# Kernel tuning notes

Hardware: AMD Instinct MI355X
Metric: run time of the kernel (lower is better)

Reference implementation:

```python
import jax, jax.numpy as jnp
import numpy as np

L_COORD = 5.0
L_NOOBJ = 0.5
S = 7  # YOLOv1 grid size


def _iou(b1, b2):
    # b1, b2: [..., 4] = (cx, cy, w, h), centers expressed in grid-cell units (divide by S)
    x1 = b1[..., 0] / S - b1[..., 2] / 2
    y1 = b1[..., 1] / S - b1[..., 3] / 2
    x2 = b1[..., 0] / S + b1[..., 2] / 2
    y2 = b1[..., 1] / S + b1[..., 3] / 2
    u1 = b2[..., 0] / S - b2[..., 2] / 2
    v1 = b2[..., 1] / S - b2[..., 3] / 2
    u2 = b2[..., 0] / S + b2[..., 2] / 2
    v2 = b2[..., 1] / S + b2[..., 3] / 2
    a1 = (x2 - x1) * (y2 - y1)
    a2 = (u2 - u1) * (v2 - v1)
    left = jnp.maximum(x1, u1)
    right = jnp.minimum(x2, u2)
    top = jnp.maximum(y1, v1)
    bottom = jnp.minimum(y2, v2)
    valid = (left < right) & (top < bottom)
    inter = jnp.where(valid, (right - left) * (bottom - top), 0.0)
    union = a1 + a2 - inter
    return jnp.where(valid, inter / union, 0.0)


def _yolo_loss(predict, label):
    # predict, label: [N, 7, 7, 26]; layout = [box1(5), box2(5), classes(16)]
    N = predict.shape[0]
    conf_lab = label[..., 4]
    coord_m = (conf_lab > 0).astype(predict.dtype)   # cells with an object
    noobj_m = (conf_lab == 0).astype(predict.dtype)  # empty cells

    # no-object cells: both predicted confidences pushed to 0
    noobj_c = jnp.sum(noobj_m * (predict[..., 4] ** 2 + predict[..., 9] ** 2))

    # class MSE on object cells
    class_loss = jnp.sum(coord_m * jnp.sum((predict[..., 10:] - label[..., 10:]) ** 2, axis=-1))

    b1 = predict[..., 0:4]
    c1 = predict[..., 4]
    b2 = predict[..., 5:9]
    c2 = predict[..., 9]
    lb = label[..., 0:4]

    iou1 = _iou(b1, lb)
    iou2 = _iou(b2, lb)
    pick1 = iou1 > iou2  # responsible box (strict >, matching torch)

    sel = jnp.where(pick1[..., None], b1, b2)  # select responsible box before sqrt
    coord_cell = (jnp.sum((sel[..., :2] - lb[..., :2]) ** 2, axis=-1)
                  + jnp.sum((jnp.sqrt(sel[..., 2:4]) - jnp.sqrt(lb[..., 2:4])) ** 2, axis=-1))
    obj_c_cell = jnp.where(pick1, (c1 - iou1) ** 2, (c2 - iou2) ** 2)
    noobj_extra = jnp.where(pick1, c2 ** 2, c1 ** 2)  # non-responsible box conf -> 0

    coord_loss = jnp.sum(coord_m * coord_cell)
    obj_c_loss = jnp.sum(coord_m * obj_c_cell)
    noobj_c = noobj_c + jnp.sum(coord_m * noobj_extra)

    return (L_COORD * coord_loss + obj_c_loss + L_NOOBJ * noobj_c + class_loss) / N


def setup_inputs() -> dict:
    key = jax.random.key(0)
    k1, k2, k3 = jax.random.split(key, 3)
    B = 8192
    # positive values so sqrt(w), sqrt(h) are well-defined (as the torch code assumes)
    predict = jax.random.uniform(k1, (B, 7, 7, 26), jnp.float32, 0.05, 1.0)
    label = jax.random.uniform(k2, (B, 7, 7, 26), jnp.float32, 0.05, 1.0)
    obj = (jax.random.uniform(k3, (B, 7, 7)) < 0.04).astype(jnp.float32)  # ~2 objects/image
    label = label.at[..., 4].set(obj)
    return {"predict": predict, "label": label}


def reference(predict, label):
    return _yolo_loss(predict, label)
```

## Files before the change

kernel.cpp:

```cpp
#include <hip/hip_runtime.h>

#define NCH 26
#define CPB 256
#define THREADS 256
#define TILE_FLOATS (CPB * NCH)
#define TILE_BYTES  (TILE_FLOATS * 4)

typedef __attribute__((address_space(3))) unsigned int  lds_u32_t;
typedef const __attribute__((address_space(1))) unsigned int glb_u32_t;

__device__ __forceinline__ float iou_pair_r(const float* b, const float* g) {
    const float inv_s = 1.0f / 7.0f;
    float x1 = b[0] * inv_s - b[2] * 0.5f;
    float y1 = b[1] * inv_s - b[3] * 0.5f;
    float x2 = b[0] * inv_s + b[2] * 0.5f;
    float y2 = b[1] * inv_s + b[3] * 0.5f;
    float u1 = g[0] * inv_s - g[2] * 0.5f;
    float v1 = g[1] * inv_s - g[3] * 0.5f;
    float u2 = g[0] * inv_s + g[2] * 0.5f;
    float v2 = g[1] * inv_s + g[3] * 0.5f;
    float a1 = (x2 - x1) * (y2 - y1);
    float a2 = (u2 - u1) * (v2 - v1);
    float left   = fmaxf(x1, u1);
    float right  = fminf(x2, u2);
    float top    = fmaxf(y1, v1);
    float bottom = fminf(y2, v2);
    bool valid = (left < right) && (top < bottom);
    float inter = valid ? (right - left) * (bottom - top) : 0.0f;
    float uni = a1 + a2 - inter;
    return valid ? inter / uni : 0.0f;
}

__global__ __launch_bounds__(THREADS) void yolo_loss_main(
        const float* __restrict__ predict,
        const float* __restrict__ label,
        float* __restrict__ partials,
        int n_cells) {
    __shared__ float sp[TILE_FLOATS];
    __shared__ float sl[TILE_FLOATS];

    const int tid = threadIdx.x;
    const int bid = blockIdx.x;
    const int wave = tid >> 6;
    const int lane = tid & 63;
    const long long base = (long long)bid * TILE_FLOATS;
    const long long total = (long long)n_cells * NCH;

    if (base + TILE_FLOATS <= total) {
        const char* gp = (const char*)(predict + base);
        const char* gl = (const char*)(label + base);
        #pragma unroll
        for (int c = 0; c < 7; ++c) {
            int chunk = wave + 4 * c;
            if (chunk < 26) {
                int off = chunk * 1024 + lane * 16;
                __builtin_amdgcn_global_load_lds(
                    (glb_u32_t*)(gp + off),
                    (lds_u32_t*)((char*)sp + off), 16, 0, 0);
                __builtin_amdgcn_global_load_lds(
                    (glb_u32_t*)(gl + off),
                    (lds_u32_t*)((char*)sl + off), 16, 0, 0);
            }
        }
    } else {
        for (int i = tid; i < TILE_FLOATS; i += THREADS) {
            long long g = base + i;
            sp[i] = (g < total) ? predict[g] : 0.0f;
            sl[i] = (g < total) ? label[g] : 0.0f;
        }
    }
    __syncthreads();

    float partial = 0.0f;
    long long cell = (long long)bid * CPB + tid;
    if (cell < n_cells) {
        float p[NCH], l[NCH];
        const float2* pv = (const float2*)&sp[tid * NCH];
        const float2* lv = (const float2*)&sl[tid * NCH];
        #pragma unroll
        for (int k = 0; k < 13; ++k) {
            float2 a = pv[k]; p[2 * k] = a.x; p[2 * k + 1] = a.y;
            float2 b = lv[k]; l[2 * k] = b.x; l[2 * k + 1] = b.y;
        }

        float conf_lab = l[4];
        float coord_m = (conf_lab > 0.0f) ? 1.0f : 0.0f;
        float noobj_m = (conf_lab == 0.0f) ? 1.0f : 0.0f;

        float acc_noobj = noobj_m * (p[4] * p[4] + p[9] * p[9]);

        float class_s = 0.0f;
        #pragma unroll
        for (int k = 10; k < 26; ++k) {
            float d = p[k] - l[k];
            class_s += d * d;
        }

        float iou1 = iou_pair_r(p + 0, l);
        float iou2 = iou_pair_r(p + 5, l);
        bool pick1 = iou1 > iou2;

        float s0 = pick1 ? p[0] : p[5];
        float s1 = pick1 ? p[1] : p[6];
        float s2 = pick1 ? p[2] : p[7];
        float s3 = pick1 ? p[3] : p[8];
        float dx = s0 - l[0];
        float dy = s1 - l[1];
        float dw = sqrtf(s2) - sqrtf(l[2]);
        float dh = sqrtf(s3) - sqrtf(l[3]);
        float coord_cell = dx * dx + dy * dy + dw * dw + dh * dh;

        float csel   = pick1 ? p[4] : p[9];
        float iousel = pick1 ? iou1 : iou2;
        float t = csel - iousel;
        float obj_c = t * t;

        float cother = pick1 ? p[9] : p[4];
        acc_noobj += coord_m * cother * cother;

        partial = 5.0f * coord_m * coord_cell
                + coord_m * obj_c
                + 0.5f * acc_noobj
                + coord_m * class_s;
    }

    #pragma unroll
    for (int off = 32; off > 0; off >>= 1)
        partial += __shfl_down(partial, off, 64);

    __shared__ float wsum[THREADS / 64];
    if ((tid & 63) == 0) wsum[tid >> 6] = partial;
    __syncthreads();
    if (tid == 0) {
        float s = 0.0f;
        #pragma unroll
        for (int w = 0; w < THREADS / 64; ++w) s += wsum[w];
        partials[bid] = s;
    }
}

__global__ __launch_bounds__(256) void yolo_loss_finalize(
        const float* __restrict__ partials, int n, float inv_n,
        float* __restrict__ out) {
    float s = 0.0f;
    for (int i = threadIdx.x; i < n; i += 256) s += partials[i];
    #pragma unroll
    for (int off = 32; off > 0; off >>= 1)
        s += __shfl_down(s, off, 64);
    __shared__ float wsum[4];
    if ((threadIdx.x & 63) == 0) wsum[threadIdx.x >> 6] = s;
    __syncthreads();
    if (threadIdx.x == 0)
        out[0] = (wsum[0] + wsum[1] + wsum[2] + wsum[3]) * inv_n;
}

extern "C" void kernel_launch(void* const* d_in, const int* in_sizes, int n_in,
                              void* d_out, int out_size, void* d_ws, size_t ws_size,
                              hipStream_t stream) {
    const float* predict = (const float*)d_in[0];
    const float* label   = (const float*)d_in[1];
    float* out = (float*)d_out;
    float* partials = (float*)d_ws;

    int total   = in_sizes[0];
    int n_cells = total / NCH;
    int N = n_cells / 49;
    int nblocks = (n_cells + CPB - 1) / CPB;

    yolo_loss_main<<<nblocks, THREADS, 0, stream>>>(predict, label, partials, n_cells);
    yolo_loss_finalize<<<1, 256, 0, stream>>>(partials, nblocks, 1.0f / (float)N, out);
}
```

Before: 101.5 us.

## Load labels directly to registers and fold finalize into atomic accumulation

Label data no longer goes through LDS. Each thread reads the label fields it needs straight from global memory into registers, skipping channels 5-9, which the loss never uses. This halves per-block LDS usage, which should let more blocks reside per CU and hide memory latency better. The separate finalize kernel is replaced by a memset plus per-block atomicAdd of the scaled partial, saving one launch but adding serialized atomics on a single address and a non-deterministic summation order.

Result: slower. 114.1 us (+12.4%).

```diff
diff --git a/kernel.cpp b/kernel.cpp
--- a/kernel.cpp
+++ b/kernel.cpp
@@ -4,7 +4,6 @@
 #define CPB 256
 #define THREADS 256
 #define TILE_FLOATS (CPB * NCH)
-#define TILE_BYTES  (TILE_FLOATS * 4)
 
 typedef __attribute__((address_space(3))) unsigned int  lds_u32_t;
 typedef const __attribute__((address_space(1))) unsigned int glb_u32_t;
@@ -34,10 +33,10 @@
 __global__ __launch_bounds__(THREADS) void yolo_loss_main(
         const float* __restrict__ predict,
         const float* __restrict__ label,
-        float* __restrict__ partials,
+        float* __restrict__ out,
+        float inv_n,
         int n_cells) {
     __shared__ float sp[TILE_FLOATS];
-    __shared__ float sl[TILE_FLOATS];
 
     const int tid = threadIdx.x;
     const int bid = blockIdx.x;
@@ -45,10 +44,10 @@
     const int lane = tid & 63;
     const long long base = (long long)bid * TILE_FLOATS;
     const long long total = (long long)n_cells * NCH;
+    const bool full_tile = (base + TILE_FLOATS <= total);
 
-    if (base + TILE_FLOATS <= total) {
+    if (full_tile) {
         const char* gp = (const char*)(predict + base);
-        const char* gl = (const char*)(label + base);
         #pragma unroll
         for (int c = 0; c < 7; ++c) {
             int chunk = wave + 4 * c;
@@ -57,30 +56,39 @@
                 __builtin_amdgcn_global_load_lds(
                     (glb_u32_t*)(gp + off),
                     (lds_u32_t*)((char*)sp + off), 16, 0, 0);
-                __builtin_amdgcn_global_load_lds(
-                    (glb_u32_t*)(gl + off),
-                    (lds_u32_t*)((char*)sl + off), 16, 0, 0);
             }
         }
     } else {
         for (int i = tid; i < TILE_FLOATS; i += THREADS) {
             long long g = base + i;
             sp[i] = (g < total) ? predict[g] : 0.0f;
-            sl[i] = (g < total) ? label[g] : 0.0f;
         }
     }
+
+    float l[NCH];
+    long long cell = (long long)bid * CPB + tid;
+    if (cell < n_cells) {
+        const float* lb = label + cell * NCH;
+        const float2* lv = (const float2*)lb;
+        float2 t0 = lv[0];  l[0] = t0.x; l[1] = t0.y;
+        float2 t1 = lv[1];  l[2] = t1.x; l[3] = t1.y;
+        l[4] = lb[4];
+        #pragma unroll
+        for (int k = 5; k < 13; ++k) {
+            float2 t = lv[k];
+            l[2 * k] = t.x; l[2 * k + 1] = t.y;
+        }
+    }
+
     __syncthreads();
 
     float partial = 0.0f;
-    long long cell = (long long)bid * CPB + tid;
     if (cell < n_cells) {
-        float p[NCH], l[NCH];
+        float p[NCH];
         const float2* pv = (const float2*)&sp[tid * NCH];
-        const float2* lv = (const float2*)&sl[tid * NCH];
         #pragma unroll
         for (int k = 0; k < 13; ++k) {
             float2 a = pv[k]; p[2 * k] = a.x; p[2 * k + 1] = a.y;
-            float2 b = lv[k]; l[2 * k] = b.x; l[2 * k + 1] = b.y;
         }
 
         float conf_lab = l[4];
@@ -135,23 +143,8 @@
         float s = 0.0f;
         #pragma unroll
         for (int w = 0; w < THREADS / 64; ++w) s += wsum[w];
-        partials[bid] = s;
+        atomicAdd(out, s * inv_n);
     }
-}
-
-__global__ __launch_bounds__(256) void yolo_loss_finalize(
-        const float* __restrict__ partials, int n, float inv_n,
-        float* __restrict__ out) {
-    float s = 0.0f;
-    for (int i = threadIdx.x; i < n; i += 256) s += partials[i];
-    #pragma unroll
-    for (int off = 32; off > 0; off >>= 1)
-        s += __shfl_down(s, off, 64);
-    __shared__ float wsum[4];
-    if ((threadIdx.x & 63) == 0) wsum[threadIdx.x >> 6] = s;
-    __syncthreads();
-    if (threadIdx.x == 0)
-        out[0] = (wsum[0] + wsum[1] + wsum[2] + wsum[3]) * inv_n;
 }
 
 extern "C" void kernel_launch(void* const* d_in, const int* in_sizes, int n_in,
@@ -160,13 +153,13 @@
     const float* predict = (const float*)d_in[0];
     const float* label   = (const float*)d_in[1];
     float* out = (float*)d_out;
-    float* partials = (float*)d_ws;
 
     int total   = in_sizes[0];
     int n_cells = total / NCH;
     int N = n_cells / 49;
     int nblocks = (n_cells + CPB - 1) / CPB;
 
-    yolo_loss_main<<<nblocks, THREADS, 0, stream>>>(predict, label, partials, n_cells);
-    yolo_loss_finalize<<<1, 256, 0, stream>>>(partials, nblocks, 1.0f / (float)N, out);
+    hipMemsetAsync(out, 0, sizeof(float) * out_size, stream);
+    yolo_loss_main<<<nblocks, THREADS, 0, stream>>>(
+        predict, label, out, 1.0f / (float)N, n_cells);
 }
```

## Use persistent single-wave blocks with double-buffered LDS prefetch of cell tiles

Applied to the files above, without the earlier changes.

Replaces the one-tile-per-block launch with a fixed grid of 768 single-wave blocks that loop over 128-cell tiles in grid-stride order. The next tile is prefetched into a second LDS buffer with direct global-to-LDS loads, waiting only for the current tile via vmcnt, so memory traffic overlaps with compute. Leftover cells are handled in the finalize kernel. It removes block-level syncthreads and per-block launch overhead, but each block has only one wave, so latency hiding depends on many resident blocks per CU and on the hand-written vmcnt count being correct.

New measurement: 105.9 us. 1.04x slower.

```diff
diff --git a/kernel.cpp b/kernel.cpp
--- a/kernel.cpp
+++ b/kernel.cpp
@@ -1,10 +1,9 @@
 #include <hip/hip_runtime.h>
 
 #define NCH 26
-#define CPB 256
-#define THREADS 256
-#define TILE_FLOATS (CPB * NCH)
-#define TILE_BYTES  (TILE_FLOATS * 4)
+#define TCELLS 128
+#define TILE_FLOATS (TCELLS * NCH)
+#define GRID_MAIN 768
 
 typedef __attribute__((address_space(3))) unsigned int  lds_u32_t;
 typedef const __attribute__((address_space(1))) unsigned int glb_u32_t;
@@ -31,119 +30,127 @@
     return valid ? inter / uni : 0.0f;
 }
 
-__global__ __launch_bounds__(THREADS) void yolo_loss_main(
+__device__ __forceinline__ float cell_loss(const float* p, const float* l) {
+    float conf_lab = l[4];
+    float coord_m = (conf_lab > 0.0f) ? 1.0f : 0.0f;
+    float noobj_m = (conf_lab == 0.0f) ? 1.0f : 0.0f;
+
+    float acc_noobj = noobj_m * (p[4] * p[4] + p[9] * p[9]);
+
+    float class_s = 0.0f;
+    #pragma unroll
+    for (int k = 10; k < 26; ++k) {
+        float d = p[k] - l[k];
+        class_s += d * d;
+    }
+
+    float iou1 = iou_pair_r(p + 0, l);
+    float iou2 = iou_pair_r(p + 5, l);
+    bool pick1 = iou1 > iou2;
+
+    float s0 = pick1 ? p[0] : p[5];
+    float s1 = pick1 ? p[1] : p[6];
+    float s2 = pick1 ? p[2] : p[7];
+    float s3 = pick1 ? p[3] : p[8];
+    float dx = s0 - l[0];
+    float dy = s1 - l[1];
+    float dw = sqrtf(s2) - sqrtf(l[2]);
+    float dh = sqrtf(s3) - sqrtf(l[3]);
+    float coord_cell = dx * dx + dy * dy + dw * dw + dh * dh;
+
+    float csel   = pick1 ? p[4] : p[9];
+    float iousel = pick1 ? iou1 : iou2;
+    float t = csel - iousel;
+    float obj_c = t * t;
+
+    float cother = pick1 ? p[9] : p[4];
+    acc_noobj += coord_m * cother * cother;
+
+    return 5.0f * coord_m * coord_cell
+         + coord_m * obj_c
+         + 0.5f * acc_noobj
+         + coord_m * class_s;
+}
+
+__global__ __launch_bounds__(64) void yolo_loss_main(
         const float* __restrict__ predict,
         const float* __restrict__ label,
         float* __restrict__ partials,
-        int n_cells) {
-    __shared__ float sp[TILE_FLOATS];
-    __shared__ float sl[TILE_FLOATS];
+        int n_tiles) {
+    __shared__ float lds[2][2][TILE_FLOATS];
+    const int lane = threadIdx.x;
+    const int bid  = blockIdx.x;
+    const int nb   = gridDim.x;
 
-    const int tid = threadIdx.x;
-    const int bid = blockIdx.x;
-    const int wave = tid >> 6;
-    const int lane = tid & 63;
-    const long long base = (long long)bid * TILE_FLOATS;
-    const long long total = (long long)n_cells * NCH;
-
-    if (base + TILE_FLOATS <= total) {
-        const char* gp = (const char*)(predict + base);
-        const char* gl = (const char*)(label + base);
+    auto stage = [&](int tile, int b) {
+        const char* gp = (const char*)(predict + (long long)tile * TILE_FLOATS);
+        const char* gl = (const char*)(label   + (long long)tile * TILE_FLOATS);
+        char* dp = (char*)&lds[b][0][0];
+        char* dl = (char*)&lds[b][1][0];
         #pragma unroll
-        for (int c = 0; c < 7; ++c) {
-            int chunk = wave + 4 * c;
-            if (chunk < 26) {
-                int off = chunk * 1024 + lane * 16;
-                __builtin_amdgcn_global_load_lds(
-                    (glb_u32_t*)(gp + off),
-                    (lds_u32_t*)((char*)sp + off), 16, 0, 0);
-                __builtin_amdgcn_global_load_lds(
-                    (glb_u32_t*)(gl + off),
-                    (lds_u32_t*)((char*)sl + off), 16, 0, 0);
-            }
+        for (int c = 0; c < 13; ++c) {
+            int off = c * 1024 + lane * 16;
+            __builtin_amdgcn_global_load_lds(
+                (glb_u32_t*)(gp + off), (lds_u32_t*)(dp + off), 16, 0, 0);
+            __builtin_amdgcn_global_load_lds(
+                (glb_u32_t*)(gl + off), (lds_u32_t*)(dl + off), 16, 0, 0);
         }
-    } else {
-        for (int i = tid; i < TILE_FLOATS; i += THREADS) {
-            long long g = base + i;
-            sp[i] = (g < total) ? predict[g] : 0.0f;
-            sl[i] = (g < total) ? label[g] : 0.0f;
-        }
-    }
-    __syncthreads();
+    };
 
     float partial = 0.0f;
-    long long cell = (long long)bid * CPB + tid;
-    if (cell < n_cells) {
-        float p[NCH], l[NCH];
-        const float2* pv = (const float2*)&sp[tid * NCH];
-        const float2* lv = (const float2*)&sl[tid * NCH];
+    int buf = 0;
+    if (bid < n_tiles) stage(bid, 0);
+
+    for (int t = bid; t < n_tiles; t += nb) {
+        int tn = t + nb;
+        if (tn < n_tiles) {
+            stage(tn, buf ^ 1);
+            asm volatile("s_waitcnt vmcnt(26)" ::: "memory");
+        } else {
+            asm volatile("s_waitcnt vmcnt(0)" ::: "memory");
+        }
+        __builtin_amdgcn_sched_barrier(0);
+
         #pragma unroll
-        for (int k = 0; k < 13; ++k) {
-            float2 a = pv[k]; p[2 * k] = a.x; p[2 * k + 1] = a.y;
-            float2 b = lv[k]; l[2 * k] = b.x; l[2 * k + 1] = b.y;
+        for (int h = 0; h < 2; ++h) {
+            int cell = lane + 64 * h;
+            float p[NCH], l[NCH];
+            const float2* pv = (const float2*)&lds[buf][0][cell * NCH];
+            const float2* lv = (const float2*)&lds[buf][1][cell * NCH];
+            #pragma unroll
+            for (int k = 0; k < 13; ++k) {
+                float2 a  = pv[k]; p[2 * k] = a.x;  p[2 * k + 1] = a.y;
+                float2 b2 = lv[k]; l[2 * k] = b2.x; l[2 * k + 1] = b2.y;
+            }
+            partial += cell_loss(p, l);
         }
-
-        float conf_lab = l[4];
-        float coord_m = (conf_lab > 0.0f) ? 1.0f : 0.0f;
-        float noobj_m = (conf_lab == 0.0f) ? 1.0f : 0.0f;
-
-        float acc_noobj = noobj_m * (p[4] * p[4] + p[9] * p[9]);
-
-        float class_s = 0.0f;
-        #pragma unroll
-        for (int k = 10; k < 26; ++k) {
-            float d = p[k] - l[k];
-            class_s += d * d;
-        }
-
-        float iou1 = iou_pair_r(p + 0, l);
-        float iou2 = iou_pair_r(p + 5, l);
-        bool pick1 = iou1 > iou2;
-
-        float s0 = pick1 ? p[0] : p[5];
-        float s1 = pick1 ? p[1] : p[6];
-        float s2 = pick1 ? p[2] : p[7];
-        float s3 = pick1 ? p[3] : p[8];
-        float dx = s0 - l[0];
-        float dy = s1 - l[1];
-        float dw = sqrtf(s2) - sqrtf(l[2]);
-        float dh = sqrtf(s3) - sqrtf(l[3]);
-        float coord_cell = dx * dx + dy * dy + dw * dw + dh * dh;
-
-        float csel   = pick1 ? p[4] : p[9];
-        float iousel = pick1 ? iou1 : iou2;
-        float t = csel - iousel;
-        float obj_c = t * t;
-
-        float cother = pick1 ? p[9] : p[4];
-        acc_noobj += coord_m * cother * cother;
-
-        partial = 5.0f * coord_m * coord_cell
-                + coord_m * obj_c
-                + 0.5f * acc_noobj
-                + coord_m * class_s;
+        buf ^= 1;
     }
 
     #pragma unroll
     for (int off = 32; off > 0; off >>= 1)
         partial += __shfl_down(partial, off, 64);
-
-    __shared__ float wsum[THREADS / 64];
-    if ((tid & 63) == 0) wsum[tid >> 6] = partial;
-    __syncthreads();
-    if (tid == 0) {
-        float s = 0.0f;
-        #pragma unroll
-        for (int w = 0; w < THREADS / 64; ++w) s += wsum[w];
-        partials[bid] = s;
-    }
+    if (lane == 0) partials[bid] = partial;
 }
 
 __global__ __launch_bounds__(256) void yolo_loss_finalize(
-        const float* __restrict__ partials, int n, float inv_n,
+        const float* __restrict__ partials, int nparts,
+        const float* __restrict__ predict,
+        const float* __restrict__ label,
+        int tail_start, int n_cells, float inv_n,
         float* __restrict__ out) {
     float s = 0.0f;
-    for (int i = threadIdx.x; i < n; i += 256) s += partials[i];
+    for (int i = threadIdx.x; i < nparts; i += 256) s += partials[i];
+
+    for (int c = tail_start + threadIdx.x; c < n_cells; c += 256) {
+        float p[NCH], l[NCH];
+        const float* pp = predict + (long long)c * NCH;
+        const float* ll = label   + (long long)c * NCH;
+        #pragma unroll
+        for (int k = 0; k < NCH; ++k) { p[k] = pp[k]; l[k] = ll[k]; }
+        s += cell_loss(p, l);
+    }
+
     #pragma unroll
     for (int off = 32; off > 0; off >>= 1)
         s += __shfl_down(s, off, 64);
@@ -165,8 +172,14 @@
     int total   = in_sizes[0];
     int n_cells = total / NCH;
     int N = n_cells / 49;
-    int nblocks = (n_cells + CPB - 1) / CPB;
+    int n_tiles = n_cells / TCELLS;
+    int tail_start = n_tiles * TCELLS;
 
-    yolo_loss_main<<<nblocks, THREADS, 0, stream>>>(predict, label, partials, n_cells);
-    yolo_loss_finalize<<<1, 256, 0, stream>>>(partials, nblocks, 1.0f / (float)N, out);
+    int grid_main = n_tiles < GRID_MAIN ? (n_tiles > 0 ? n_tiles : 1) : GRID_MAIN;
+
+    yolo_loss_main<<<grid_main, 64, 0, stream>>>(predict, label, partials, n_tiles);
+    yolo_loss_finalize<<<1, 256, 0, stream>>>(partials, grid_main,
+                                              predict, label,
+                                              tail_start, n_cells,
+                                              1.0f / (float)N, out);
 }
```
